# Optimization experiments

Hardware: AMD Instinct MI355X
Metric: run time of the kernel (lower is better)

Reference implementation:

```python
import jax, jax.numpy as jnp
import numpy as np

BLANK = 1   # Offsets.GO
NEG = -1e30  # effective -inf that stays finite under logaddexp


def setup_inputs() -> dict:
    key = jax.random.key(0)
    k1, k2, k3, k4 = jax.random.split(key, 4)
    T, B, V, S = 1000, 64, 512, 100
    logits = jax.random.normal(k1, (T, B, V), dtype=jnp.float32)
    log_prob = jax.nn.log_softmax(logits, axis=-1)  # ctc_loss expects log-probs
    input_lengths = jax.random.randint(k2, (B,), T // 2, T + 1, dtype=jnp.int32)
    # target tokens avoid PAD(0)/GO(1,blank)/EOS(2), matching the masked_select semantics
    targets = jax.random.randint(k3, (B, S), 3, V, dtype=jnp.int32)
    target_lengths = jax.random.randint(k4, (B,), S // 2, S + 1, dtype=jnp.int32)
    return {"log_prob": log_prob, "input_lengths": input_lengths,
            "targets": targets, "target_lengths": target_lengths}


def _ctc_loss_sum(log_prob, input_lengths, targets, target_lengths):
    # log_prob: (T, B, V) log-softmax outputs; targets: (B, S) padded labels
    T, B, V = log_prob.shape
    S = targets.shape[1]
    Se = 2 * S + 1  # extended label sequence: blank-interleaved

    ext = jnp.full((B, Se), BLANK, dtype=targets.dtype).at[:, 1::2].set(targets)
    pos = jnp.arange(Se)
    ext_len = 2 * target_lengths + 1                      # (B,)
    valid = pos[None, :] < ext_len[:, None]               # (B, Se)
    ext_m2 = jnp.pad(ext[:, :-2], ((0, 0), (2, 0)), constant_values=BLANK)
    allow_skip = (ext != BLANK) & (ext != ext_m2) & (pos[None, :] >= 2)

    # emit[t, b, s] = log_prob[t, b, ext[b, s]]  -> (T, B, Se)
    emit = jnp.take_along_axis(log_prob, jnp.broadcast_to(ext[None], (T, B, Se)), axis=2)

    # alpha init at t=0
    alpha = jnp.full((B, Se), NEG, dtype=log_prob.dtype)
    alpha = alpha.at[:, 0].set(emit[0, :, 0])
    alpha = alpha.at[:, 1].set(jnp.where(target_lengths > 0, emit[0, :, 1], NEG))
    alpha = jnp.where(valid, alpha, NEG)

    def step(alpha, xt):
        emit_t, t = xt
        a1 = alpha
        a2 = jnp.pad(alpha[:, :-1], ((0, 0), (1, 0)), constant_values=NEG)
        a3 = jnp.where(allow_skip,
                       jnp.pad(alpha[:, :-2], ((0, 0), (2, 0)), constant_values=NEG),
                       NEG)
        new = jnp.logaddexp(jnp.logaddexp(a1, a2), a3) + emit_t
        new = jnp.where(valid, new, NEG)
        # freeze alpha once past each sample's input length
        alpha = jnp.where((t < input_lengths)[:, None], new, alpha)
        return alpha, None

    alpha, _ = jax.lax.scan(step, alpha, (emit[1:], jnp.arange(1, T)))

    last = 2 * target_lengths  # index of trailing blank in extended sequence
    a_last = jnp.take_along_axis(alpha, last[:, None], axis=1)[:, 0]
    a_prev = jnp.take_along_axis(alpha, jnp.maximum(last - 1, 0)[:, None], axis=1)[:, 0]
    loglik = jnp.logaddexp(a_last, a_prev)
    loss = -loglik
    # zero_infinity=True: infeasible alignments contribute 0
    loss = jnp.where(loglik < 0.5 * NEG, 0.0, loss)
    return jnp.sum(loss)  # reduction='sum'


def reference(log_prob, input_lengths, targets, target_lengths):
    return _ctc_loss_sum(log_prob, input_lengths, targets, target_lengths)
```

## Files before the change

kernel.cpp:

```cpp
#include <hip/hip_runtime.h>


#define NEGF (-1e30f)

constexpr int CT_T  = 1000;
constexpr int CT_B  = 64;
constexpr int CT_V  = 512;
constexpr int CT_S  = 100;
constexpr int CT_Se = 201;
constexpr float LOG2E = 1.4426950408889634f;
constexpr float LN2   = 0.6931471805599453f;
constexpr float SHIFT = 5.0f;

typedef float f4 __attribute__((ext_vector_type(4)));

#if __has_builtin(__builtin_amdgcn_exp2f) && __has_builtin(__builtin_amdgcn_logf)
__device__ __forceinline__ float fexp2(float x) { return __builtin_amdgcn_exp2f(x); }
__device__ __forceinline__ float flog2(float x) { return __builtin_amdgcn_logf(x); }
__device__ __forceinline__ float frcp(float x)  { return __builtin_amdgcn_rcpf(x); }
#else
__device__ __forceinline__ float fexp2(float x) { return exp2f(x); }
__device__ __forceinline__ float flog2(float x) { return log2f(x); }
__device__ __forceinline__ float frcp(float x)  { return 1.0f / x; }
#endif

__device__ __forceinline__ float lae2_b2(float x, float y) {
    float m = fmaxf(x, y);
    float d = fminf(x, y) - m;
    return m + flog2(1.0f + fexp2(d));
}
__device__ __forceinline__ float lae3_b2(float x, float y, float z) {
    float m = fmaxf(fmaxf(x, y), z);
    float s = fexp2(x - m) + fexp2(y - m) + fexp2(z - m);
    return m + flog2(s);
}

__device__ __forceinline__ float wave_shr1(float x) {
    return __int_as_float(__builtin_amdgcn_update_dpp(
        0, __float_as_int(x), 0x138, 0xf, 0xf, true));
}
__device__ __forceinline__ float wave_max_nonneg(float x) {
#define DPPMAX(ctrl) x = fmaxf(x, __int_as_float(__builtin_amdgcn_update_dpp( \
        0, __float_as_int(x), ctrl, 0xf, 0xf, true)))
    DPPMAX(0x111); DPPMAX(0x112); DPPMAX(0x114); DPPMAX(0x118);
    DPPMAX(0x142); DPPMAX(0x143);
#undef DPPMAX
    return __int_as_float(__builtin_amdgcn_readlane(__float_as_int(x), 63));
}

typedef const __attribute__((address_space(1))) unsigned int* as1_uint_ptr;
typedef __attribute__((address_space(3))) unsigned int* as3_uint_ptr;
__device__ __forceinline__ void gld16(const void* g, void* l) {
    __builtin_amdgcn_global_load_lds((as1_uint_ptr)g, (as3_uint_ptr)l, 16, 0, 0);
}

__global__ __launch_bounds__(256, 1) void ctc_alpha(
    const float* __restrict__ logp,
    const int*   __restrict__ in_len,
    const int*   __restrict__ tgt,
    const int*   __restrict__ tgt_len,
    float*       __restrict__ loss_ws)
{
    __shared__ __align__(16) float sr[3][8][CT_V];
    __shared__ __align__(16) float cp[2][8][256];

    const int b    = blockIdx.x;
    const int tid  = threadIdx.x;
    const int wv   = tid >> 6;
    const int lane = tid & 63;
    const int Tin  = in_len[b];
    const int Lt   = tgt_len[b];
    const int lim  = 2 * Lt + 1;
    const int* tg  = tgt + b * CT_S;

    const int K = (Tin - 1 + 7) / 8;

    const int s0 = 4 * lane, s1 = s0 + 1, s3 = s0 + 3;
    const int i1 = min((s1 - 1) >> 1, CT_S - 1);
    const int i3 = min((s3 - 1) >> 1, CT_S - 1);
    const int c1 = tg[i1];
    const int c3 = tg[i3];
    const float sk1 = ((s1 >= 3) && (s1 < CT_Se) && (c1 != tg[max(i1 - 1, 0)])) ? 1.f : 0.f;
    const float sk3 = ((s3 >= 3) && (s3 < CT_Se) && (c3 != tg[max(i3 - 1, 0)])) ? 1.f : 0.f;
    const float m0 = (s0     < lim) ? 1.f : 0.f;
    const float m1 = (s0 + 1 < lim) ? 1.f : 0.f;
    const float m2 = (s0 + 2 < lim) ? 1.f : 0.f;
    const float m3 = (s0 + 3 < lim) ? 1.f : 0.f;

    float a0 = 0.f, a1 = 0.f, a2 = 0.f, a3 = 0.f, pa3 = 0.f;
    if (tid == 0) {
        const float* r0 = logp + (size_t)b * CT_V;
        a0 = fexp2(fmaf(r0[1], LOG2E, SHIFT));
        if (Lt > 0) a1 = fexp2(fmaf(r0[c1], LOG2E, SHIFT));
    }
    float rs = 0.f;

    auto issue = [&](int k) {
        const int tb = 1 + 8 * k;
        const int buf = k % 3;
        #pragma unroll
        for (int i = 0; i < 8; ++i) {
            const int t = min(tb + i, CT_T - 1);
            const char* g = (const char*)(logp + ((size_t)t * CT_B + b) * CT_V)
                          + (size_t)lane * 16;
            gld16(g,        &sr[buf][i][0]);
            gld16(g + 1024, &sr[buf][i][256]);
        }
    };

    auto pgather = [&](int c) {
        asm volatile("s_waitcnt vmcnt(0)" ::: "memory");
        __builtin_amdgcn_sched_barrier(0);
        const int sb = c % 3, cb = c & 1;
        #pragma unroll
        for (int i = 0; i < 8; ++i) {
            float gb = sr[sb][i][1];
            float g1 = sr[sb][i][c1];
            float g3 = sr[sb][i][c3];
            f4 v;
            v.x = fexp2(fmaf(gb, LOG2E, SHIFT));
            v.y = fexp2(fmaf(g1, LOG2E, SHIFT));
            v.z = fexp2(fmaf(g3, LOG2E, SHIFT));
            v.w = 0.f;
            reinterpret_cast<f4*>(&cp[cb][i][0])[lane] = v;
        }
        asm volatile("s_waitcnt lgkmcnt(0)" ::: "memory");
        __builtin_amdgcn_sched_barrier(0);
    };

    auto renorm = [&]() {
        float lm = wave_max_nonneg(fmaxf(fmaxf(a0, a1), fmaxf(a2, a3)));
        if (lm > 0.f) {
            float sc = frcp(lm);
            rs += flog2(lm);
            a0 *= sc; a1 *= sc; a2 *= sc; a3 *= sc;
            pa3 = wave_shr1(a3);
        }
    };

    auto run8 = [&](int cb, int tb, bool guard) {
        unsigned base = (unsigned)(size_t)(&cp[cb][0][0]) + 16u * (unsigned)lane;
        f4 e[8];
        asm volatile(
            "ds_read_b128 %0, %8 offset:0\n\t"
            "ds_read_b128 %1, %8 offset:1024\n\t"
            "ds_read_b128 %2, %8 offset:2048\n\t"
            "ds_read_b128 %3, %8 offset:3072\n\t"
            "ds_read_b128 %4, %8 offset:4096\n\t"
            "ds_read_b128 %5, %8 offset:5120\n\t"
            "ds_read_b128 %6, %8 offset:6144\n\t"
            "ds_read_b128 %7, %8 offset:7168\n\t"
            "s_waitcnt lgkmcnt(0)"
            : "=&v"(e[0]), "=&v"(e[1]), "=&v"(e[2]), "=&v"(e[3]),
              "=&v"(e[4]), "=&v"(e[5]), "=&v"(e[6]), "=&v"(e[7])
            : "v"(base));
        #pragma unroll
        for (int i = 0; i < 8; ++i) {
            float ex = e[i].x * m0, ey = e[i].y * m1;
            float ez = e[i].x * m2, ew = e[i].z * m3;
            float n0 = (a0 + pa3) * ex;
            float n1 = fmaf(sk1, pa3, a1 + a0) * ey;
            float n2 = (a2 + a1) * ez;
            float n3 = fmaf(sk3, a1, a3 + a2) * ew;
            if (!guard || (tb + i < Tin)) { a0 = n0; a1 = n1; a2 = n2; a3 = n3; }
            pa3 = wave_shr1(a3);
        }
    };

    if (wv) {
        const int p = wv - 1;
        if (p < K) issue(p);
        if (p == 0) pgather(0);
    }
    __builtin_amdgcn_s_barrier();

    for (int j = 0; j < K; ++j) {
        if (wv == 0) {
            run8(j & 1, 1 + 8 * j, j == K - 1);
            if (j & 1) renorm();
        } else {
            const int p = wv - 1;
            if (((j + 1) % 3) == p && (j + 1) < K) pgather(j + 1);
            if ((j % 3) == p && (j + 3) < K) issue(j + 3);
        }
        __builtin_amdgcn_s_barrier();
    }

    if (wv) {
        asm volatile("s_waitcnt vmcnt(0)" ::: "memory");
        return;
    }

    const int last = 2 * Lt;
    const int prev = max(last - 1, 0);
    const int lr = last & 3, lidx = last >> 2;
    float av = (lr == 0) ? a0 : (lr == 1) ? a1 : (lr == 2) ? a2 : a3;
    float a_last = __shfl(av, lidx);
    const int pr = prev & 3, pidx = prev >> 2;
    float pv = (pr == 0) ? a0 : (pr == 1) ? a1 : (pr == 2) ? a2 : a3;
    float a_prev = __shfl(pv, pidx);

    float sum = a_last + a_prev;
    float loss = 0.f;
    if (sum > 0.f)
        loss = -(flog2(sum) + rs - SHIFT * (float)Tin) * LN2;
    if (lane == 0) loss_ws[b] = loss;
}

__global__ __launch_bounds__(64) void ctc_alpha_fb(
    const float* __restrict__ logp, const int* __restrict__ in_len,
    const int* __restrict__ tgt, const int* __restrict__ tgt_len,
    float* __restrict__ loss_ws)
{
    const int b = blockIdx.x, lane = threadIdx.x;
    const int Tin = in_len[b], Lt = tgt_len[b];
    const int ext_len = 2 * Lt + 1;
    const int* tg = tgt + b * CT_S;
    const int s0 = 4 * lane, s1 = s0 + 1, s3 = s0 + 3;
    const int i1 = min((s1 - 1) >> 1, CT_S - 1);
    const int i3 = min((s3 - 1) >> 1, CT_S - 1);
    const int c1 = tg[i1], c3 = tg[i3];
    const bool skip1 = (s1 >= 3) && (s1 < CT_Se) && (c1 != tg[max(i1 - 1, 0)]);
    const bool skip3 = (s3 >= 3) && (s3 < CT_Se) && (c3 != tg[max(i3 - 1, 0)]);
    const bool v0 = s0 < ext_len, v1 = s1 < ext_len;
    const bool v2 = (s0 + 2) < ext_len, v3 = s3 < ext_len;
    const float* row0 = logp + (long long)b * CT_V;
    const long long stride = (long long)CT_B * CT_V;
    float a0 = NEGF, a1 = NEGF, a2 = NEGF, a3 = NEGF;
    if (lane == 0) {
        a0 = row0[1] * LOG2E;
        if (ext_len > 1) a1 = row0[c1] * LOG2E;
    }
    float3 E0, E1, E2, E3;
    auto ld = [&](float3& e, int t) {
        int tt = min(t, CT_T - 1);
        const float* r = row0 + (long long)tt * stride;
        e.x = r[1] * LOG2E; e.y = r[c1] * LOG2E; e.z = r[c3] * LOG2E;
    };
    auto step = [&](const float3& e) {
        float pa3 = __shfl_up(a3, 1);
        if (lane == 0) pa3 = NEGF;
        float z1 = skip1 ? pa3 : NEGF;
        float z3 = skip3 ? a1 : NEGF;
        float n0 = v0 ? lae2_b2(a0, pa3)    + e.x : NEGF;
        float n1 = v1 ? lae3_b2(a1, a0, z1) + e.y : NEGF;
        float n2 = v2 ? lae2_b2(a2, a1)     + e.x : NEGF;
        float n3 = v3 ? lae3_b2(a3, a2, z3) + e.z : NEGF;
        a0 = n0; a1 = n1; a2 = n2; a3 = n3;
    };
    ld(E0, 1); ld(E1, 2); ld(E2, 3); ld(E3, 4);
    for (int t = 1; t < Tin; t += 4) {
        step(E0); ld(E0, t + 4);
        if (t + 1 < Tin) { step(E1); ld(E1, t + 5); }
        if (t + 2 < Tin) { step(E2); ld(E2, t + 6); }
        if (t + 3 < Tin) { step(E3); ld(E3, t + 7); }
    }
    const int last = 2 * Lt, prev = max(last - 1, 0);
    const int lr = last & 3, lidx = last >> 2;
    float av = (lr == 0) ? a0 : (lr == 1) ? a1 : (lr == 2) ? a2 : a3;
    float a_last = __shfl(av, lidx);
    const int pr = prev & 3, pidx = prev >> 2;
    float pv = (pr == 0) ? a0 : (pr == 1) ? a1 : (pr == 2) ? a2 : a3;
    float a_prev = __shfl(pv, pidx);
    float loglik = lae2_b2(a_last, a_prev) * LN2;
    float loss = (loglik < 0.5f * NEGF) ? 0.0f : -loglik;
    if (lane == 0) loss_ws[b] = loss;
}

__global__ __launch_bounds__(64) void ctc_sum(const float* __restrict__ loss_ws,
                                              float* __restrict__ out)
{
    float v = loss_ws[threadIdx.x];
    #pragma unroll
    for (int o = 32; o > 0; o >>= 1) v += __shfl_down(v, o);
    if (threadIdx.x == 0) out[0] = v;
}

extern "C" void kernel_launch(void* const* d_in, const int* in_sizes, int n_in,
                              void* d_out, int out_size, void* d_ws, size_t ws_size,
                              hipStream_t stream) {
    const float* logp    = (const float*)d_in[0];
    const int*   in_len  = (const int*)d_in[1];
    const int*   tgt     = (const int*)d_in[2];
    const int*   tgt_len = (const int*)d_in[3];
    float* out = (float*)d_out;
    float* loss_ws = (float*)d_ws;

    if (ws_size >= 256 * sizeof(float)) {
        hipLaunchKernelGGL(ctc_alpha, dim3(CT_B), dim3(256), 0, stream,
                           logp, in_len, tgt, tgt_len, loss_ws);
    } else {
        hipLaunchKernelGGL(ctc_alpha_fb, dim3(CT_B), dim3(64), 0, stream,
                           logp, in_len, tgt, tgt_len, loss_ws);
    }
    hipLaunchKernelGGL(ctc_sum, dim3(1), dim3(64), 0, stream, loss_ws, out);
}
```

Baseline: 216.7 us.

## Split producer waves across timestep rows and use partial vmcnt waits

Before, each producer wave loaded and gathered a whole 8-timestep chunk in round-robin turns. Now all three producer waves share every chunk by row range (3/3/2 rows), issue loads three chunks ahead, and wait with partial vmcnt counts so older chunks can be consumed while newer loads are still in flight. The validity masks are folded into the gathered emission values on the producer side, which shortens the consumer's serial recurrence. The guarded final chunk is peeled out of the loop. The hand-counted vmcnt thresholds are fragile and must match the per-wave load counts exactly.

```diff
diff --git a/kernel.cpp b/kernel.cpp
--- a/kernel.cpp
+++ b/kernel.cpp
@@ -53,6 +53,11 @@
 __device__ __forceinline__ void gld16(const void* g, void* l) {
     __builtin_amdgcn_global_load_lds((as1_uint_ptr)g, (as3_uint_ptr)l, 16, 0, 0);
 }
+
+#define WAIT_VM(n) do { \
+    asm volatile("s_waitcnt vmcnt(" #n ")" ::: "memory"); \
+    __builtin_amdgcn_sched_barrier(0); } while (0)
+#define DRAIN_LGKM() asm volatile("s_waitcnt lgkmcnt(0)" ::: "memory")
 
 __global__ __launch_bounds__(256, 1) void ctc_alpha(
     const float* __restrict__ logp,
@@ -87,6 +92,10 @@
     const float m2 = (s0 + 2 < lim) ? 1.f : 0.f;
     const float m3 = (s0 + 3 < lim) ? 1.f : 0.f;
 
+    const int p  = wv - 1;
+    const int rb = p * 3;
+    const int re = (p == 2) ? 8 : rb + 3;
+
     float a0 = 0.f, a1 = 0.f, a2 = 0.f, a3 = 0.f, pa3 = 0.f;
     if (tid == 0) {
         const float* r0 = logp + (size_t)b * CT_V;
@@ -95,11 +104,10 @@
     }
     float rs = 0.f;
 
-    auto issue = [&](int k) {
+    auto iss = [&](int k) {
         const int tb = 1 + 8 * k;
         const int buf = k % 3;
-        #pragma unroll
-        for (int i = 0; i < 8; ++i) {
+        for (int i = rb; i < re; ++i) {
             const int t = min(tb + i, CT_T - 1);
             const char* g = (const char*)(logp + ((size_t)t * CT_B + b) * CT_V)
                           + (size_t)lane * 16;
@@ -109,23 +117,19 @@
     };
 
     auto pgather = [&](int c) {
-        asm volatile("s_waitcnt vmcnt(0)" ::: "memory");
-        __builtin_amdgcn_sched_barrier(0);
         const int sb = c % 3, cb = c & 1;
-        #pragma unroll
-        for (int i = 0; i < 8; ++i) {
+        for (int i = rb; i < re; ++i) {
             float gb = sr[sb][i][1];
             float g1 = sr[sb][i][c1];
             float g3 = sr[sb][i][c3];
+            float eb = fexp2(fmaf(gb, LOG2E, SHIFT));
             f4 v;
-            v.x = fexp2(fmaf(gb, LOG2E, SHIFT));
-            v.y = fexp2(fmaf(g1, LOG2E, SHIFT));
-            v.z = fexp2(fmaf(g3, LOG2E, SHIFT));
-            v.w = 0.f;
+            v.x = eb * m0;
+            v.y = fexp2(fmaf(g1, LOG2E, SHIFT)) * m1;
+            v.z = eb * m2;
+            v.w = fexp2(fmaf(g3, LOG2E, SHIFT)) * m3;
             reinterpret_cast<f4*>(&cp[cb][i][0])[lane] = v;
         }
-        asm volatile("s_waitcnt lgkmcnt(0)" ::: "memory");
-        __builtin_amdgcn_sched_barrier(0);
     };
 
     auto renorm = [&]() {
@@ -156,32 +160,37 @@
             : "v"(base));
         #pragma unroll
         for (int i = 0; i < 8; ++i) {
-            float ex = e[i].x * m0, ey = e[i].y * m1;
-            float ez = e[i].x * m2, ew = e[i].z * m3;
-            float n0 = (a0 + pa3) * ex;
-            float n1 = fmaf(sk1, pa3, a1 + a0) * ey;
-            float n2 = (a2 + a1) * ez;
-            float n3 = fmaf(sk3, a1, a3 + a2) * ew;
+            float n0 = (a0 + pa3) * e[i].x;
+            float n1 = fmaf(sk1, pa3, a1 + a0) * e[i].y;
+            float n2 = (a2 + a1) * e[i].z;
+            float n3 = fmaf(sk3, a1, a3 + a2) * e[i].w;
             if (!guard || (tb + i < Tin)) { a0 = n0; a1 = n1; a2 = n2; a3 = n3; }
             pa3 = wave_shr1(a3);
         }
     };
 
     if (wv) {
-        const int p = wv - 1;
-        if (p < K) issue(p);
-        if (p == 0) pgather(0);
+        WAIT_VM(0);
+        iss(0); iss(1); iss(2);
+        if (p == 2) { WAIT_VM(8); } else { WAIT_VM(12); }
+        pgather(0);
+        DRAIN_LGKM();
     }
     __builtin_amdgcn_s_barrier();
 
-    for (int j = 0; j < K; ++j) {
+    for (int j = 0; j < K - 1; ++j) {
         if (wv == 0) {
-            run8(j & 1, 1 + 8 * j, j == K - 1);
+            run8(j & 1, 1 + 8 * j, false);
             if (j & 1) renorm();
         } else {
-            const int p = wv - 1;
-            if (((j + 1) % 3) == p && (j + 1) < K) pgather(j + 1);
-            if ((j % 3) == p && (j + 3) < K) issue(j + 3);
+            if (j + 1 < K) {
+                if (j + 1 == K - 1)      { WAIT_VM(0); }
+                else if (p == 2)         { WAIT_VM(4); }
+                else                     { WAIT_VM(6); }
+                pgather(j + 1);
+            }
+            if (j + 3 < K) iss(j + 3);
+            DRAIN_LGKM();
         }
         __builtin_amdgcn_s_barrier();
     }
@@ -190,6 +199,8 @@
         asm volatile("s_waitcnt vmcnt(0)" ::: "memory");
         return;
     }
+
+    run8((K - 1) & 1, 1 + 8 * (K - 1), true);
 
     const int last = 2 * Lt;
     const int prev = max(last - 1, 0);
```

Result: slower. 229.2 us (+5.8%).

## Ping-pong alpha recursion between two waves with per-lane gathered LDS staging

Applied to the files above, without the earlier changes.

Replaces the full-row LDS staging plus a separate gather/exp wave with per-lane 4-byte global-to-LDS loads of only the three needed columns. Two compute waves now alternate: one runs 16 recursion steps while the other reads its staged data and computes the exps into registers. Alpha state and the running log-scale are handed between the two waves through shared memory each tile. Masks are folded into the exponent shift to save multiplies. This is meant to shorten the serial critical path and cut staging bandwidth, at the cost of a handoff through LDS and a barrier per tile, plus more register pressure.

```diff
diff --git a/kernel.cpp b/kernel.cpp
--- a/kernel.cpp
+++ b/kernel.cpp
@@ -53,16 +53,24 @@
 __device__ __forceinline__ void gld16(const void* g, void* l) {
     __builtin_amdgcn_global_load_lds((as1_uint_ptr)g, (as3_uint_ptr)l, 16, 0, 0);
 }
-
-__global__ __launch_bounds__(256, 1) void ctc_alpha(
+__device__ __forceinline__ void gld4(const void* g, void* l) {
+    __builtin_amdgcn_global_load_lds((as1_uint_ptr)g, (as3_uint_ptr)l, 4, 0, 0);
+}
+
+#define WAIT_VM0() do { \
+    asm volatile("s_waitcnt vmcnt(0)" ::: "memory"); \
+    __builtin_amdgcn_sched_barrier(0); } while (0)
+#define DRAIN_LGKM() asm volatile("s_waitcnt lgkmcnt(0)" ::: "memory")
+
+__global__ __launch_bounds__(256, 1) void ctc_alpha_pp(
     const float* __restrict__ logp,
     const int*   __restrict__ in_len,
     const int*   __restrict__ tgt,
     const int*   __restrict__ tgt_len,
     float*       __restrict__ loss_ws)
 {
-    __shared__ __align__(16) float sr[3][8][CT_V];
-    __shared__ __align__(16) float cp[2][8][256];
+    __shared__ __align__(16) float stage[8][8][192];
+    __shared__ __align__(16) float hand[272];
 
     const int b    = blockIdx.x;
     const int tid  = threadIdx.x;
@@ -73,7 +81,8 @@
     const int lim  = 2 * Lt + 1;
     const int* tg  = tgt + b * CT_S;
 
-    const int K = (Tin - 1 + 7) / 8;
+    const int K  = (Tin - 1 + 7) / 8;
+    const int NT = (Tin - 1 + 15) / 16;
 
     const int s0 = 4 * lane, s1 = s0 + 1, s3 = s0 + 3;
     const int i1 = min((s1 - 1) >> 1, CT_S - 1);
@@ -83,9 +92,9 @@
     const float sk1 = ((s1 >= 3) && (s1 < CT_Se) && (c1 != tg[max(i1 - 1, 0)])) ? 1.f : 0.f;
     const float sk3 = ((s3 >= 3) && (s3 < CT_Se) && (c3 != tg[max(i3 - 1, 0)])) ? 1.f : 0.f;
     const float m0 = (s0     < lim) ? 1.f : 0.f;
-    const float m1 = (s0 + 1 < lim) ? 1.f : 0.f;
     const float m2 = (s0 + 2 < lim) ? 1.f : 0.f;
-    const float m3 = (s0 + 3 < lim) ? 1.f : 0.f;
+    const float Sy = (s0 + 1 < lim) ? SHIFT : -1000.f;
+    const float Sw = (s0 + 3 < lim) ? SHIFT : -1000.f;
 
     float a0 = 0.f, a1 = 0.f, a2 = 0.f, a3 = 0.f, pa3 = 0.f;
     if (tid == 0) {
@@ -95,37 +104,71 @@
     }
     float rs = 0.f;
 
-    auto issue = [&](int k) {
-        const int tb = 1 + 8 * k;
-        const int buf = k % 3;
+    float ex[16], ey[16], ez[16], ew[16];
+
+    auto issue = [&](int c) {
+        if (c >= K) return;
+        const int buf = c & 7, tb = 1 + 8 * c;
         #pragma unroll
         for (int i = 0; i < 8; ++i) {
             const int t = min(tb + i, CT_T - 1);
-            const char* g = (const char*)(logp + ((size_t)t * CT_B + b) * CT_V)
-                          + (size_t)lane * 16;
-            gld16(g,        &sr[buf][i][0]);
-            gld16(g + 1024, &sr[buf][i][256]);
-        }
-    };
-
-    auto pgather = [&](int c) {
-        asm volatile("s_waitcnt vmcnt(0)" ::: "memory");
+            const float* r = logp + ((size_t)t * CT_B + b) * CT_V;
+            gld4(r + c1, &stage[buf][i][0]);
+            gld4(r + c3, &stage[buf][i][64]);
+            gld4(r + 1,  &stage[buf][i][128]);
+        }
+    };
+
+    auto read24 = [&](int c, float (&g)[24]) {
+        unsigned base = (unsigned)(size_t)(&stage[c & 7][0][0]) + 4u * (unsigned)lane;
+        asm volatile(
+            "ds_read_b32 %0,  %24 offset:0\n\t"
+            "ds_read_b32 %1,  %24 offset:256\n\t"
+            "ds_read_b32 %2,  %24 offset:512\n\t"
+            "ds_read_b32 %3,  %24 offset:768\n\t"
+            "ds_read_b32 %4,  %24 offset:1024\n\t"
+            "ds_read_b32 %5,  %24 offset:1280\n\t"
+            "ds_read_b32 %6,  %24 offset:1536\n\t"
+            "ds_read_b32 %7,  %24 offset:1792\n\t"
+            "ds_read_b32 %8,  %24 offset:2048\n\t"
+            "ds_read_b32 %9,  %24 offset:2304\n\t"
+            "ds_read_b32 %10, %24 offset:2560\n\t"
+            "ds_read_b32 %11, %24 offset:2816\n\t"
+            "ds_read_b32 %12, %24 offset:3072\n\t"
+            "ds_read_b32 %13, %24 offset:3328\n\t"
+            "ds_read_b32 %14, %24 offset:3584\n\t"
+            "ds_read_b32 %15, %24 offset:3840\n\t"
+            "ds_read_b32 %16, %24 offset:4096\n\t"
+            "ds_read_b32 %17, %24 offset:4352\n\t"
+            "ds_read_b32 %18, %24 offset:4608\n\t"
+            "ds_read_b32 %19, %24 offset:4864\n\t"
+            "ds_read_b32 %20, %24 offset:5120\n\t"
+            "ds_read_b32 %21, %24 offset:5376\n\t"
+            "ds_read_b32 %22, %24 offset:5632\n\t"
+            "ds_read_b32 %23, %24 offset:5888\n\t"
+            "s_waitcnt lgkmcnt(0)"
+            : "=&v"(g[0]), "=&v"(g[1]), "=&v"(g[2]), "=&v"(g[3]), "=&v"(g[4]),
+              "=&v"(g[5]), "=&v"(g[6]), "=&v"(g[7]), "=&v"(g[8]), "=&v"(g[9]),
+              "=&v"(g[10]), "=&v"(g[11]), "=&v"(g[12]), "=&v"(g[13]),
+              "=&v"(g[14]), "=&v"(g[15]), "=&v"(g[16]), "=&v"(g[17]),
+              "=&v"(g[18]), "=&v"(g[19]), "=&v"(g[20]), "=&v"(g[21]),
+              "=&v"(g[22]), "=&v"(g[23])
+            : "v"(base));
         __builtin_amdgcn_sched_barrier(0);
-        const int sb = c % 3, cb = c & 1;
+    };
+
+    auto prep2 = [&](int c0) {
+        float gA[24], gB[24];
+        read24(c0, gA);
+        read24(c0 + 1, gB);
         #pragma unroll
-        for (int i = 0; i < 8; ++i) {
-            float gb = sr[sb][i][1];
-            float g1 = sr[sb][i][c1];
-            float g3 = sr[sb][i][c3];
-            f4 v;
-            v.x = fexp2(fmaf(gb, LOG2E, SHIFT));
-            v.y = fexp2(fmaf(g1, LOG2E, SHIFT));
-            v.z = fexp2(fmaf(g3, LOG2E, SHIFT));
-            v.w = 0.f;
-            reinterpret_cast<f4*>(&cp[cb][i][0])[lane] = v;
-        }
-        asm volatile("s_waitcnt lgkmcnt(0)" ::: "memory");
-        __builtin_amdgcn_sched_barrier(0);
+        for (int s = 0; s < 16; ++s) {
+            const float* g = (s < 8) ? &gA[3 * s] : &gB[3 * (s - 8)];
+            float e1 = fexp2(fmaf(g[0], LOG2E, Sy));
+            float e3 = fexp2(fmaf(g[1], LOG2E, Sw));
+            float eb = fexp2(fmaf(g[2], LOG2E, SHIFT));
+            ex[s] = eb * m0; ey[s] = e1; ez[s] = eb * m2; ew[s] = e3;
+        }
     };
 
     auto renorm = [&]() {
@@ -138,58 +181,54 @@
         }
     };
 
-    auto run8 = [&](int cb, int tb, bool guard) {
-        unsigned base = (unsigned)(size_t)(&cp[cb][0][0]) + 16u * (unsigned)lane;
-        f4 e[8];
-        asm volatile(
-            "ds_read_b128 %0, %8 offset:0\n\t"
-            "ds_read_b128 %1, %8 offset:1024\n\t"
-            "ds_read_b128 %2, %8 offset:2048\n\t"
-            "ds_read_b128 %3, %8 offset:3072\n\t"
-            "ds_read_b128 %4, %8 offset:4096\n\t"
-            "ds_read_b128 %5, %8 offset:5120\n\t"
-            "ds_read_b128 %6, %8 offset:6144\n\t"
-            "ds_read_b128 %7, %8 offset:7168\n\t"
-            "s_waitcnt lgkmcnt(0)"
-            : "=&v"(e[0]), "=&v"(e[1]), "=&v"(e[2]), "=&v"(e[3]),
-              "=&v"(e[4]), "=&v"(e[5]), "=&v"(e[6]), "=&v"(e[7])
-            : "v"(base));
+    auto recurse = [&](int i) {
+        if (i > 0) {
+            f4 h = *reinterpret_cast<f4*>(&hand[4 * lane]);
+            a0 = h.x; a1 = h.y; a2 = h.z; a3 = h.w;
+            rs = hand[256];
+            pa3 = wave_shr1(a3);
+        }
+        const int tb = 1 + 16 * i;
+        const bool guard = (16 * i + 16 > Tin - 1);
         #pragma unroll
-        for (int i = 0; i < 8; ++i) {
-            float ex = e[i].x * m0, ey = e[i].y * m1;
-            float ez = e[i].x * m2, ew = e[i].z * m3;
-            float n0 = (a0 + pa3) * ex;
-            float n1 = fmaf(sk1, pa3, a1 + a0) * ey;
-            float n2 = (a2 + a1) * ez;
-            float n3 = fmaf(sk3, a1, a3 + a2) * ew;
-            if (!guard || (tb + i < Tin)) { a0 = n0; a1 = n1; a2 = n2; a3 = n3; }
+        for (int s = 0; s < 16; ++s) {
+            float n0 = (a0 + pa3) * ex[s];
+            float n1 = fmaf(sk1, pa3, a1 + a0) * ey[s];
+            float n2 = (a2 + a1) * ez[s];
+            float n3 = fmaf(sk3, a1, a3 + a2) * ew[s];
+            if (!guard || (tb + s < Tin)) { a0 = n0; a1 = n1; a2 = n2; a3 = n3; }
             pa3 = wave_shr1(a3);
         }
-    };
-
-    if (wv) {
-        const int p = wv - 1;
-        if (p < K) issue(p);
-        if (p == 0) pgather(0);
-    }
+        renorm();
+        f4 h; h.x = a0; h.y = a1; h.z = a2; h.w = a3;
+        *reinterpret_cast<f4*>(&hand[4 * lane]) = h;
+        if (lane == 0) hand[256] = rs;
+        DRAIN_LGKM();
+    };
+
+    if (wv == 2) { WAIT_VM0(); issue(0); issue(1); issue(2); issue(3); WAIT_VM0(); }
+    else if (wv == 3) { WAIT_VM0(); issue(4); issue(5); }
     __builtin_amdgcn_s_barrier();
-
-    for (int j = 0; j < K; ++j) {
-        if (wv == 0) {
-            run8(j & 1, 1 + 8 * j, j == K - 1);
-            if (j & 1) renorm();
+    if (wv == 0) prep2(0);
+    __builtin_amdgcn_s_barrier();
+
+    for (int i = 0; i < NT; ++i) {
+        if (wv < 2) {
+            if ((i & 1) == wv)      recurse(i);
+            else if (i + 1 < NT)    prep2(2 * i + 2);
         } else {
-            const int p = wv - 1;
-            if (((j + 1) % 3) == p && (j + 1) < K) pgather(j + 1);
-            if ((j % 3) == p && (j + 3) < K) issue(j + 3);
+            const int p = wv - 2;
+            if ((i & 1) == p) { issue(2 * i + 6); issue(2 * i + 7); }
+            else              { WAIT_VM0(); }
         }
         __builtin_amdgcn_s_barrier();
     }
 
-    if (wv) {
+    if (wv >= 2) {
         asm volatile("s_waitcnt vmcnt(0)" ::: "memory");
         return;
     }
+    if (wv != ((NT - 1) & 1)) return;
 
     const int last = 2 * Lt;
     const int prev = max(last - 1, 0);
@@ -287,7 +326,7 @@
     float* loss_ws = (float*)d_ws;
 
     if (ws_size >= 256 * sizeof(float)) {
-        hipLaunchKernelGGL(ctc_alpha, dim3(CT_B), dim3(256), 0, stream,
+        hipLaunchKernelGGL(ctc_alpha_pp, dim3(CT_B), dim3(256), 0, stream,
                            logp, in_len, tgt, tgt_len, loss_ws);
     } else {
         hipLaunchKernelGGL(ctc_alpha_fb, dim3(CT_B), dim3(64), 0, stream,
```

Measured after the change: 203.1 us (median of 2 runs). 6.3% less time.
